# Performance work log

Measured on AMD Instinct MI355X. Metric: run time of the kernel, lower is better.

The kernel has to match this reference:

```python
import jax, jax.numpy as jnp
import numpy as np
import math

NUM_BUCKETS = 32
MAX_DISTANCE = 128

def _next_pow2(n):
    return 1 << (int(n) - 1).bit_length()

def _rel_pos_bucket(rel_pos):
    # causal T5 bucket: n = max(q - k, 0)
    n = jnp.maximum(-rel_pos, 0)
    max_exact = NUM_BUCKETS // 2
    is_small = n < max_exact
    n_safe = jnp.maximum(n, 1).astype(jnp.float32)
    val_if_large = max_exact + (
        jnp.log(n_safe / max_exact) / math.log(MAX_DISTANCE / max_exact) * (NUM_BUCKETS - max_exact)
    ).astype(jnp.int32)
    val_if_large = jnp.minimum(val_if_large, NUM_BUCKETS - 1)
    return jnp.where(is_small, n, val_if_large)

def setup_inputs() -> dict:
    key = jax.random.key(0)
    ks = jax.random.split(key, 20)
    B, L, D = 8, 2048, 128
    H, DQK, DV = 16, 64, 256
    s = 0.05
    return {
        'x': jax.random.normal(ks[0], (B, L, D), jnp.float32),
        'expansion': jax.random.normal(ks[1], (H, D), jnp.float32) * s,
        'reduction': jax.random.normal(ks[2], (H, D), jnp.float32) * s,
        'alphas': jax.random.normal(ks[3], (H,), jnp.float32),
        'dampen_factors': jax.random.normal(ks[4], (H,), jnp.float32),
        'rel_bias': jax.random.normal(ks[5], (NUM_BUCKETS, 1), jnp.float32) * s,
        'W_qk': jax.random.normal(ks[6], (D, DQK), jnp.float32) * s,
        'b_qk': jnp.zeros((DQK,), jnp.float32),
        'gamma': jax.random.normal(ks[7], (2, DQK), jnp.float32) * 0.02 + 1.0,
        'beta': jnp.zeros((2, DQK), jnp.float32),
        'W_v': jax.random.normal(ks[8], (D, DV), jnp.float32) * s,
        'b_v': jnp.zeros((DV,), jnp.float32),
        'W_reset': jax.random.normal(ks[9], (D, DV), jnp.float32) * s,
        'b_reset': jnp.zeros((DV,), jnp.float32),
        'W_update': jax.random.normal(ks[10], (D, D), jnp.float32) * s,
        'b_update': jnp.zeros((D,), jnp.float32),
        'Wh': jax.random.normal(ks[11], (D, D), jnp.float32) * s,
        'Uh': jax.random.normal(ks[12], (DV, D), jnp.float32) * s,
        'bh': jnp.zeros((D,), jnp.float32),
    }

def reference(x, expansion, reduction, alphas, dampen_factors, rel_bias,
              W_qk, b_qk, gamma, beta, W_v, b_v, W_reset, b_reset,
              W_update, b_update, Wh, Uh, bh):
    B, L, D = x.shape
    DQK = W_qk.shape[1]
    # ---- MultiHeadedEMA (causal, FFT conv) ----
    xe = jnp.einsum('bnd,hd->bnhd', x, expansion)  # [B,L,H,D]
    a = jax.nn.sigmoid(alphas)
    damp = jax.nn.sigmoid(dampen_factors)
    t = jnp.arange(L, dtype=x.dtype)
    kern = a[:, None] * ((1.0 - a) * damp)[:, None] ** t[None, :]  # [H,L]
    fft_len = _next_pow2(2 * L - 1)
    Xf = jnp.fft.rfft(xe, n=fft_len, axis=1)           # [B,F,H,D]
    Kf = jnp.fft.rfft(kern, n=fft_len, axis=-1)        # [H,F]
    y = jnp.fft.irfft(Xf * Kf.T[None, :, :, None], n=fft_len, axis=1)[:, :L]
    ema = jnp.einsum('bnhd,hd->bnd', y, reduction)     # [B,L,D]
    # ---- SingleHeadedAttention(ema, v_input=x) ----
    qk = jax.nn.silu(ema @ W_qk + b_qk)                # [B,L,DQK]
    q = qk * gamma[0] + beta[0]
    k = qk * gamma[1] + beta[1]
    v = jax.nn.silu(x @ W_v + b_v)                     # [B,L,DV]
    scale = D ** -0.5
    sim = jnp.einsum('bid,bjd->bij', q, k) * scale
    pos = jnp.arange(L)
    rel = pos[None, :] - pos[:, None]                  # [L,L] j - i
    bias = rel_bias[_rel_pos_bucket(rel), 0] * (DQK ** 0.5)
    sim = sim + bias
    sim = jnp.where(rel > 0, jnp.finfo(sim.dtype).min, sim)  # strict causal mask
    attn = jax.nn.softmax(sim, axis=-1)
    attn_out = jnp.einsum('bij,bjd->bid', attn, v)     # [B,L,DV]
    # ---- gating ----
    reset_gate = jax.nn.silu(ema @ W_reset + b_reset)
    update_gate = jax.nn.sigmoid(ema @ W_update + b_update)
    gated = attn_out * reset_gate
    Hh = jax.nn.silu(ema @ Wh + gated @ Uh + bh)
    return update_gate * Hh + (1.0 - update_gate) * x
```

## Files before the change

### kernel.cpp

```cpp
#include <hip/hip_runtime.h>
#include <hip/hip_bf16.h>
#include <math.h>

#define BB 8
#define LL 2048
#define DD 128
#define DQKN 64
#define DVN 256
#define MTOT (BB*LL)
#define SCALE 0.08838834764831845f
#define LOG2E 1.4426950408889634f
#define QSCALE (SCALE*LOG2E)

#define CHUNK 32
#define NCH (LL/CHUNK)
#define CT 4
#define NCHK 144

typedef __attribute__((ext_vector_type(4))) float f32x4;
typedef __attribute__((ext_vector_type(8))) short s16x8;

__device__ __forceinline__ float sigmoidf_(float x){ return 1.f/(1.f+__expf(-x)); }
__device__ __forceinline__ float siluf_(float x){ return x/(1.f+__expf(-x)); }
__device__ __forceinline__ __hip_bfloat16 f2bf(float f){ return __float2bfloat16(f); }
__device__ __forceinline__ ushort f2bfu(float f){ __hip_bfloat16 h = __float2bfloat16(f); return *(const ushort*)&h; }
__device__ __forceinline__ float bf2f(ushort u){ union{unsigned i; float f;} v; v.i = ((unsigned)u)<<16; return v.f; }

__device__ __forceinline__ void gl_lds16(const __hip_bfloat16* g, void* l) {
    __builtin_amdgcn_global_load_lds(
        (const __attribute__((address_space(1))) void*)g,
        (__attribute__((address_space(3))) void*)l, 16, 0, 0);
}

__global__ void pack_all(const float* __restrict__ Wqk, const float* __restrict__ Wv,
                         const float* __restrict__ Wrst, const float* __restrict__ Wu,
                         const float* __restrict__ Wh, const float* __restrict__ Uh,
                         const float* __restrict__ rel_bias,
                         __hip_bfloat16* __restrict__ WqkP, __hip_bfloat16* __restrict__ WvP,
                         __hip_bfloat16* __restrict__ WrstP, __hip_bfloat16* __restrict__ WuP,
                         __hip_bfloat16* __restrict__ WhP, __hip_bfloat16* __restrict__ UhP,
                         float* __restrict__ btab) {
    int blk = blockIdx.x;
    int l = threadIdx.x;
    if (blk == 272) {
        for (int n = l; n < LL; n += 64) {
            int bucket;
            if (n < 16) bucket = n;
            else {
                float v = logf((float)n * (1.0f/16.0f)) * (1.0f/logf(8.0f)) * 16.0f;
                bucket = 16 + (int)v;
                if (bucket > 31) bucket = 31;
            }
            btab[n] = rel_bias[bucket] * 8.0f * LOG2E;
        }
        return;
    }
    const float* W; __hip_bfloat16* Wp; int K, N;
    if (blk < 16)       { W=Wqk;  Wp=WqkP;  K=128; N=64; }
    else if (blk < 80)  { W=Wv;   Wp=WvP;   K=128; N=256; blk-=16; }
    else if (blk < 144) { W=Wrst; Wp=WrstP; K=128; N=256; blk-=80; }
    else if (blk < 176) { W=Wu;   Wp=WuP;   K=128; N=128; blk-=144; }
    else if (blk < 208) { W=Wh;   Wp=WhP;   K=128; N=128; blk-=176; }
    else                { W=Uh;   Wp=UhP;   K=256; N=128; blk-=208; }
    int k32 = blk % (K/32), n16 = blk / (K/32);
    int col = n16*16 + (l & 15);
    int krow = k32*32 + (l >> 4)*8;
    ushort tmp[8];
    #pragma unroll
    for (int j = 0; j < 8; ++j) tmp[j] = f2bfu(W[(size_t)(krow + j)*N + col]);
    *reinterpret_cast<uint4*>(Wp + ((size_t)blk*64 + l)*8) = *reinterpret_cast<uint4*>(tmp);
}

__global__ __launch_bounds__(256) void ema_scanA(const float* __restrict__ x,
                                                 const float* __restrict__ alphas,
                                                 const float* __restrict__ damps,
                                                 float* __restrict__ sl) {
    int tid = blockIdx.x * 256 + threadIdx.x;
    int d = tid & 127;
    int c = (tid >> 7) & (NCH - 1);
    int b = tid >> 13;
    float u[16], r[16];
    #pragma unroll
    for (int h = 0; h < 16; ++h) {
        float a = sigmoidf_(alphas[h]);
        r[h] = (1.f - a) * sigmoidf_(damps[h]);
        u[h] = 0.f;
    }
    const float* xp = x + ((size_t)b * LL + c * CHUNK) * DD + d;
    #pragma unroll 4
    for (int i = 0; i < CHUNK; ++i) {
        float xv = xp[(size_t)i * DD];
        #pragma unroll
        for (int h = 0; h < 16; ++h) u[h] = fmaf(r[h], u[h], xv);
    }
    float* slp = sl + ((size_t)b * NCH + c) * 16 * DD + d;
    #pragma unroll
    for (int h = 0; h < 16; ++h) slp[(size_t)h * DD] = u[h];
}

__global__ __launch_bounds__(256) void ema_scanB(const float* __restrict__ alphas,
                                                 const float* __restrict__ damps,
                                                 const float* __restrict__ sl,
                                                 float* __restrict__ carry) {
    int tid = blockIdx.x * 256 + threadIdx.x;
    int d = tid & 127;
    int h = (tid >> 7) & 15;
    int b = tid >> 11;
    float a = sigmoidf_(alphas[h]);
    float r = (1.f - a) * sigmoidf_(damps[h]);
    float rC = r;
    #pragma unroll
    for (int q = 0; q < 5; ++q) rC *= rC;
    const float* slp = sl + ((size_t)b * NCH * 16 + h) * DD + d;
    float* cp = carry + ((size_t)b * NCH * 16 + h) * DD + d;
    float u = 0.f;
    for (int c = 0; c < NCH; ++c) {
        cp[(size_t)c * 16 * DD] = u;
        u = slp[(size_t)c * 16 * DD] + rC * u;
    }
}

__global__ __launch_bounds__(256) void ema_scanC(const float* __restrict__ x,
                                                 const float* __restrict__ expansion,
                                                 const float* __restrict__ reduction,
                                                 const float* __restrict__ alphas,
                                                 const float* __restrict__ damps,
                                                 const float* __restrict__ carry,
                                                 __hip_bfloat16* __restrict__ emab,
                                                 __hip_bfloat16* __restrict__ xb) {
    int tid = blockIdx.x * 256 + threadIdx.x;
    int d = tid & 127;
    int c = (tid >> 7) & (NCH - 1);
    int b = tid >> 13;
    float u[16], r[16], we[16];
    #pragma unroll
    for (int h = 0; h < 16; ++h) {
        float a = sigmoidf_(alphas[h]);
        r[h] = (1.f - a) * sigmoidf_(damps[h]);
        we[h] = reduction[h * DD + d] * a * expansion[h * DD + d];
        u[h] = carry[((size_t)b * NCH + c) * 16 * DD + (size_t)h * DD + d];
    }
    const float* xp = x + ((size_t)b * LL + c * CHUNK) * DD + d;
    __hip_bfloat16* ep = emab + ((size_t)b * LL + c * CHUNK) * DD + d;
    __hip_bfloat16* xbp = xb + ((size_t)b * LL + c * CHUNK) * DD + d;
    #pragma unroll 4
    for (int i = 0; i < CHUNK; ++i) {
        float xv = xp[(size_t)i * DD];
        float acc = 0.f;
        #pragma unroll
        for (int h = 0; h < 16; ++h) {
            u[h] = fmaf(r[h], u[h], xv);
            acc = fmaf(we[h], u[h], acc);
        }
        ep[(size_t)i * DD] = f2bf(acc);
        xbp[(size_t)i * DD] = f2bf(xv);
    }
}

__global__ __launch_bounds__(256) void gemm_qk(const __hip_bfloat16* __restrict__ A,
        const __hip_bfloat16* __restrict__ Wp, const float* __restrict__ bias,
        const float* __restrict__ gamma, const float* __restrict__ beta,
        __hip_bfloat16* __restrict__ qb, __hip_bfloat16* __restrict__ kb) {
    __shared__ char AsB[64*256];
    const int row0 = blockIdx.x * 64;
    const int t = threadIdx.x, w = t>>6, lane = t&63, l16 = lane&15, l4 = lane>>4;
    #pragma unroll
    for (int p = 0; p < 4; ++p) {
        int idx = p*256 + t;
        int row = idx / 16, u = idx % 16;
        uint4 d = *reinterpret_cast<const uint4*>(A + (size_t)(row0+row)*DD + u*8);
        *reinterpret_cast<uint4*>(AsB + row*256 + ((u*16) ^ ((row&7)<<4))) = d;
    }
    __syncthreads();
    f32x4 acc[4];
    #pragma unroll
    for (int n = 0; n < 4; ++n) acc[n] = (f32x4){0.f,0.f,0.f,0.f};
    const int arow = w*16 + l16;
    #pragma unroll
    for (int k32 = 0; k32 < 4; ++k32) {
        s16x8 af = *reinterpret_cast<const s16x8*>(AsB + arow*256 + ((k32*64 + l4*16) ^ ((arow&7)<<4)));
        #pragma unroll
        for (int n = 0; n < 4; ++n) {
            s16x8 bfr = *reinterpret_cast<const s16x8*>(Wp + ((size_t)(n*4 + k32)*64 + lane)*8);
            acc[n] = __builtin_amdgcn_mfma_f32_16x16x32_bf16(af, bfr, acc[n], 0, 0, 0);
        }
    }
    #pragma unroll
    for (int n = 0; n < 4; ++n) {
        int col = n*16 + l16;
        float bb = bias[col];
        float g0 = gamma[col], g1 = gamma[DQKN + col];
        float be0 = beta[col], be1 = beta[DQKN + col];
        #pragma unroll
        for (int r = 0; r < 4; ++r) {
            int row = w*16 + l4*4 + r;
            float s = siluf_(acc[n][r] + bb);
            qb[(size_t)(row0+row)*DQKN + col] = f2bf((s*g0 + be0) * QSCALE);
            kb[(size_t)(row0+row)*DQKN + col] = f2bf(s*g1 + be1);
        }
    }
}

__global__ __launch_bounds__(256) void gemm_vrst(const __hip_bfloat16* __restrict__ xb,
        const __hip_bfloat16* __restrict__ emab,
        const __hip_bfloat16* __restrict__ WvP, const __hip_bfloat16* __restrict__ WrstP,
        const float* __restrict__ b_v, const float* __restrict__ b_rst,
        __hip_bfloat16* __restrict__ vT, __hip_bfloat16* __restrict__ rstb) {
    __shared__ char AsB[64*256];
    const int mode = blockIdx.y;
    const __hip_bfloat16* A = mode ? emab : xb;
    const __hip_bfloat16* Wp = mode ? WrstP : WvP;
    const float* bias = mode ? b_rst : b_v;
    const int row0 = blockIdx.x * 64;
    const int t = threadIdx.x, w = t>>6, lane = t&63, l16 = lane&15, l4 = lane>>4;
    #pragma unroll
    for (int p = 0; p < 4; ++p) {
        int idx = p*256 + t;
        int row = idx / 16, u = idx % 16;
        uint4 d = *reinterpret_cast<const uint4*>(A + (size_t)(row0+row)*DD + u*8);
        *reinterpret_cast<uint4*>(AsB + row*256 + ((u*16) ^ ((row&7)<<4))) = d;
    }
    __syncthreads();
    f32x4 acc[16];
    #pragma unroll
    for (int n = 0; n < 16; ++n) acc[n] = (f32x4){0.f,0.f,0.f,0.f};
    const int arow = w*16 + l16;
    #pragma unroll
    for (int k32 = 0; k32 < 4; ++k32) {
        s16x8 af = *reinterpret_cast<const s16x8*>(AsB + arow*256 + ((k32*64 + l4*16) ^ ((arow&7)<<4)));
        #pragma unroll
        for (int n = 0; n < 16; ++n) {
            s16x8 bfr = *reinterpret_cast<const s16x8*>(Wp + ((size_t)(n*4 + k32)*64 + lane)*8);
            acc[n] = __builtin_amdgcn_mfma_f32_16x16x32_bf16(af, bfr, acc[n], 0, 0, 0);
        }
    }
    if (mode == 0) {
        int bb_i = row0 >> 11;
        int lpos0 = (row0 & 2047) + w*16 + l4*4;
        #pragma unroll
        for (int n = 0; n < 16; ++n) {
            int col = n*16 + l16;
            float bb = bias[col];
            ushort pk[4];
            #pragma unroll
            for (int r = 0; r < 4; ++r) pk[r] = f2bfu(siluf_(acc[n][r] + bb));
            *reinterpret_cast<ushort4*>(vT + ((size_t)bb_i*DVN + col)*LL + lpos0) = *reinterpret_cast<ushort4*>(pk);
        }
    } else {
        #pragma unroll
        for (int n = 0; n < 16; ++n) {
            int col = n*16 + l16;
            float bb = bias[col];
            #pragma unroll
            for (int r = 0; r < 4; ++r) {
                int row = w*16 + l4*4 + r;
                rstb[(size_t)(row0+row)*DVN + col] = f2bf(siluf_(acc[n][r] + bb));
            }
        }
    }
}

__global__ __launch_bounds__(256) void attn_kernel(
    const __hip_bfloat16* __restrict__ qg, const __hip_bfloat16* __restrict__ kg,
    const __hip_bfloat16* __restrict__ vTg, const float* __restrict__ btab,
    __hip_bfloat16* __restrict__ aob, __hip_bfloat16* __restrict__ part_o,
    float* __restrict__ part_ml) {
    __shared__ __hip_bfloat16 Ks[2][64 * 64];
    __shared__ __hip_bfloat16 Vs[2][256 * 64];
    __shared__ __hip_bfloat16 Ps[4][16][72];
    __shared__ float btl[320];
    const int cid = NCHK - 1 - (int)blockIdx.x;
    const int b = blockIdx.y;
    int g = 0;
    while (cid >= 2*(g+1)*(g+2)) ++g;
    const int rel = cid - 2*g*(g+1);
    const int ti = 4*g + rel/(g+1);
    const int cch = rel % (g+1);
    const int i0 = ti * 64;
    const int jlo = cch * (CT*64);
    int jhi = jlo + CT*64; { int je = (ti+1)*64; if (jhi > je) jhi = je; }
    const int nt = (jhi - jlo) >> 6;
    const int t = threadIdx.x;
    const int w = t >> 6, lane = t & 63;
    const int l16 = lane & 15, l4 = lane >> 4;
    char* KsB = (char*)Ks;
    char* VsB = (char*)Vs;

    const int dminE = i0 - jhi + 1;
    const int cnt = (i0 + 63 - jlo) - dminE + 1;
    for (int idx = t; idx < cnt; idx += 256) {
        int dlt = dminE + idx;
        btl[idx] = (dlt >= 0) ? btab[dlt] : -1e30f;
    }

    const int irow = i0 + w * 16 + l16;
    s16x8 qf[2];
    qf[0] = *reinterpret_cast<const s16x8*>(qg + ((size_t)b * LL + irow) * DQKN + l4 * 8);
    qf[1] = *reinterpret_cast<const s16x8*>(qg + ((size_t)b * LL + irow) * DQKN + 32 + l4 * 8);

    f32x4 o[16];
    #pragma unroll
    for (int n16 = 0; n16 < 16; ++n16) o[n16] = (f32x4){0.f, 0.f, 0.f, 0.f};
    float m[4] = {-1e30f, -1e30f, -1e30f, -1e30f};
    float l[4] = {0.f, 0.f, 0.f, 0.f};

    #define STAGE(BUF, J0) { \
        _Pragma("unroll") for (int i = 0; i < 2; ++i) { \
            int base = w * 128 + i * 64; \
            int idx = base + lane; \
            int row = idx >> 3; \
            int c16 = (idx & 7) ^ (row & 7); \
            gl_lds16(kg + ((size_t)b * LL + (J0) + row) * DQKN + c16 * 8, KsB + (BUF)*8192 + base * 16); } \
        _Pragma("unroll") for (int i = 0; i < 8; ++i) { \
            int base = w * 512 + i * 64; \
            int idx = base + lane; \
            int n = idx >> 3; \
            int c16 = (idx & 7) ^ (n & 7); \
            gl_lds16(vTg + ((size_t)b * DVN + n) * LL + (J0) + c16 * 8, VsB + (BUF)*32768 + base * 16); } }

    STAGE(0, jlo);
    __syncthreads();

    for (int tt = 0; tt < nt; ++tt) {
        const int j0 = jlo + tt * 64;
        const int cur = tt & 1;
        if (tt + 1 < nt) STAGE(cur ^ 1, j0 + 64);
        f32x4 s[4];
        #pragma unroll
        for (int t16 = 0; t16 < 4; ++t16) s[t16] = (f32x4){0.f, 0.f, 0.f, 0.f};
        #pragma unroll
        for (int c = 0; c < 2; ++c) {
            #pragma unroll
            for (int t16 = 0; t16 < 4; ++t16) {
                int j = t16 * 16 + l16;
                s16x8 kf = *reinterpret_cast<const s16x8*>(KsB + cur*8192 + j * 128 + ((c * 64 + l4 * 16) ^ ((j & 7) << 4)));
                s[t16] = __builtin_amdgcn_mfma_f32_16x16x32_bf16(qf[c], kf, s[t16], 0, 0, 0);
            }
        }
        const int Cb = (i0 + w * 16 + l4 * 4) - (j0 + l16) - dminE;
        float sv[4][4];
        float rmax[4] = {-1e30f, -1e30f, -1e30f, -1e30f};
        #pragma unroll
        for (int t16 = 0; t16 < 4; ++t16) {
            #pragma unroll
            for (int r = 0; r < 4; ++r) {
                float val = s[t16][r] + btl[Cb + r - t16 * 16];
                sv[t16][r] = val;
                rmax[r] = fmaxf(rmax[r], val);
            }
        }
        #pragma unroll
        for (int off = 1; off < 16; off <<= 1) {
            #pragma unroll
            for (int r = 0; r < 4; ++r) rmax[r] = fmaxf(rmax[r], __shfl_xor(rmax[r], off));
        }
        bool need = (rmax[0] > m[0]) || (rmax[1] > m[1]) || (rmax[2] > m[2]) || (rmax[3] > m[3]);
        if (__any(need)) {
            float alpha[4];
            #pragma unroll
            for (int r = 0; r < 4; ++r) {
                float mn = fmaxf(m[r], rmax[r]);
                alpha[r] = exp2f(m[r] - mn);
                m[r] = mn;
                l[r] *= alpha[r];
            }
            #pragma unroll
            for (int n16 = 0; n16 < 16; ++n16) {
                #pragma unroll
                for (int r = 0; r < 4; ++r) o[n16][r] *= alpha[r];
            }
        }
        float psum[4] = {0.f, 0.f, 0.f, 0.f};
        #pragma unroll
        for (int t16 = 0; t16 < 4; ++t16) {
            #pragma unroll
            for (int r = 0; r < 4; ++r) {
                float p = exp2f(sv[t16][r] - m[r]);
                psum[r] += p;
                Ps[w][l4 * 4 + r][t16 * 16 + l16] = f2bf(p);
            }
        }
        #pragma unroll
        for (int off = 1; off < 16; off <<= 1) {
            #pragma unroll
            for (int r = 0; r < 4; ++r) psum[r] += __shfl_xor(psum[r], off);
        }
        #pragma unroll
        for (int r = 0; r < 4; ++r) l[r] += psum[r];
        #pragma unroll
        for (int c = 0; c < 2; ++c) {
            s16x8 pf = *reinterpret_cast<const s16x8*>(&Ps[w][l16][c * 32 + l4 * 8]);
            #pragma unroll
            for (int n16 = 0; n16 < 16; ++n16) {
                int n = n16 * 16 + l16;
                s16x8 vf = *reinterpret_cast<const s16x8*>(VsB + cur*32768 + n * 128 + ((c * 64 + l4 * 16) ^ ((n & 7) << 4)));
                o[n16] = __builtin_amdgcn_mfma_f32_16x16x32_bf16(pf, vf, o[n16], 0, 0, 0);
            }
        }
        __syncthreads();
    }
    #undef STAGE
    if (ti < 4) {
        float invl[4];
        #pragma unroll
        for (int r = 0; r < 4; ++r) invl[r] = 1.f / l[r];
        #pragma unroll
        for (int n16 = 0; n16 < 16; ++n16) {
            #pragma unroll
            for (int r = 0; r < 4; ++r) {
                aob[((size_t)b * LL + i0 + w * 16 + l4 * 4 + r) * DVN + n16 * 16 + l16] = f2bf(o[n16][r] * invl[r]);
            }
        }
    } else {
        const size_t slot = (size_t)b * NCHK + cid;
        __hip_bfloat16* po = part_o + slot * (64 * 256);
        #pragma unroll
        for (int n16 = 0; n16 < 16; ++n16) {
            #pragma unroll
            for (int r = 0; r < 4; ++r)
                po[(size_t)(w * 16 + l4 * 4 + r) * 256 + n16 * 16 + l16] = f2bf(o[n16][r]);
        }
        if (l16 == 0) {
            #pragma unroll
            for (int r = 0; r < 4; ++r) {
                int row = w * 16 + l4 * 4 + r;
                part_ml[slot * 128 + row * 2]     = m[r];
                part_ml[slot * 128 + row * 2 + 1] = l[r];
            }
        }
    }
}

__global__ __launch_bounds__(256) void attn_combine(const __hip_bfloat16* __restrict__ part_o,
                                                    const float* __restrict__ part_ml,
                                                    __hip_bfloat16* __restrict__ aob) {
    const int ti = 4 + (int)blockIdx.x;
    const int ch = blockIdx.y;
    const int b = blockIdx.z;
    const int g = ti >> 2;
    const int nc = g + 1;
    const int cid0 = 2*g*(g+1) + (ti - 4*g)*(g+1);
    const size_t slot0 = (size_t)b * NCHK + cid0;
    __shared__ float sW[8][64];
    __shared__ float sinvL[64];
    const int t = threadIdx.x;
    if (t < 64) {
        float M = -1e30f;
        for (int c = 0; c < nc; ++c)
            M = fmaxf(M, part_ml[(slot0 + c) * 128 + t * 2]);
        float L = 0.f;
        for (int c = 0; c < nc; ++c) {
            float wv = exp2f(part_ml[(slot0 + c) * 128 + t * 2] - M);
            sW[c][t] = wv;
            L += wv * part_ml[(slot0 + c) * 128 + t * 2 + 1];
        }
        sinvL[t] = 1.f / L;
    }
    __syncthreads();
    const int i0 = ti * 64;
    #pragma unroll
    for (int it = 0; it < 4; ++it) {
        int idx = it * 256 + t;
        int row = idx >> 4, c8 = idx & 15;
        int colu = ch * 16 + c8;
        float acc[8] = {0.f,0.f,0.f,0.f,0.f,0.f,0.f,0.f};
        for (int c = 0; c < nc; ++c) {
            float wv = sW[c][row];
            uint4 d = *reinterpret_cast<const uint4*>(part_o + (slot0 + c) * (size_t)(64*256) + row * 256 + colu * 8);
            const ushort* pp = (const ushort*)&d;
            #pragma unroll
            for (int j = 0; j < 8; ++j) acc[j] = fmaf(wv, bf2f(pp[j]), acc[j]);
        }
        float il = sinvL[row];
        ushort pk[8];
        #pragma unroll
        for (int j = 0; j < 8; ++j) pk[j] = f2bfu(acc[j] * il);
        *reinterpret_cast<uint4*>(aob + ((size_t)b * LL + i0 + row) * DVN + colu * 8) = *reinterpret_cast<uint4*>(pk);
    }
}

__global__ __launch_bounds__(256) void final_mfma(
        const __hip_bfloat16* __restrict__ emab, const __hip_bfloat16* __restrict__ aob,
        const __hip_bfloat16* __restrict__ rstb, const float* __restrict__ x,
        const __hip_bfloat16* __restrict__ WhP, const __hip_bfloat16* __restrict__ UhP,
        const __hip_bfloat16* __restrict__ WuP, const float* __restrict__ bh,
        const float* __restrict__ bu, float* __restrict__ out) {
    __shared__ char As1[64*256];
    __shared__ char As2[64*512];
    const int row0 = blockIdx.x * 64;
    const int ch = blockIdx.y;
    const int t = threadIdx.x, w = t>>6, lane = t&63, l16 = lane&15, l4 = lane>>4;
    #pragma unroll
    for (int p = 0; p < 4; ++p) {
        int idx = p*256 + t;
        int row = idx / 16, u = idx % 16;
        uint4 d = *reinterpret_cast<const uint4*>(emab + (size_t)(row0+row)*DD + u*8);
        *reinterpret_cast<uint4*>(As1 + row*256 + ((u*16) ^ ((row&7)<<4))) = d;
    }
    #pragma unroll
    for (int p = 0; p < 8; ++p) {
        int idx = p*256 + t;
        int row = idx / 32, u = idx % 32;
        uint4 da = *reinterpret_cast<const uint4*>(aob + (size_t)(row0+row)*DVN + u*8);
        uint4 dr = *reinterpret_cast<const uint4*>(rstb + (size_t)(row0+row)*DVN + u*8);
        const ushort* pa = (const ushort*)&da;
        const ushort* pr = (const ushort*)&dr;
        ushort gg[8];
        #pragma unroll
        for (int j = 0; j < 8; ++j) gg[j] = f2bfu(bf2f(pa[j]) * bf2f(pr[j]));
        *reinterpret_cast<uint4*>(As2 + row*512 + ((u*16) ^ ((row&7)<<4))) = *reinterpret_cast<uint4*>(gg);
    }
    __syncthreads();
    f32x4 acc1[4], acc2[4];
    #pragma unroll
    for (int n = 0; n < 4; ++n) { acc1[n] = (f32x4){0.f,0.f,0.f,0.f}; acc2[n] = (f32x4){0.f,0.f,0.f,0.f}; }
    const int arow = w*16 + l16;
    #pragma unroll
    for (int k32 = 0; k32 < 4; ++k32) {
        s16x8 af = *reinterpret_cast<const s16x8*>(As1 + arow*256 + ((k32*64 + l4*16) ^ ((arow&7)<<4)));
        #pragma unroll
        for (int n = 0; n < 4; ++n) {
            s16x8 bw = *reinterpret_cast<const s16x8*>(WhP + ((size_t)((ch*4+n)*4 + k32)*64 + lane)*8);
            acc1[n] = __builtin_amdgcn_mfma_f32_16x16x32_bf16(af, bw, acc1[n], 0, 0, 0);
            s16x8 bu2 = *reinterpret_cast<const s16x8*>(WuP + ((size_t)((ch*4+n)*4 + k32)*64 + lane)*8);
            acc2[n] = __builtin_amdgcn_mfma_f32_16x16x32_bf16(af, bu2, acc2[n], 0, 0, 0);
        }
    }
    #pragma unroll
    for (int k32 = 0; k32 < 8; ++k32) {
        s16x8 gf = *reinterpret_cast<const s16x8*>(As2 + arow*512 + ((k32*64 + l4*16) ^ ((arow&7)<<4)));
        #pragma unroll
        for (int n = 0; n < 4; ++n) {
            s16x8 bw = *reinterpret_cast<const s16x8*>(UhP + ((size_t)((ch*4+n)*8 + k32)*64 + lane)*8);
            acc1[n] = __builtin_amdgcn_mfma_f32_16x16x32_bf16(gf, bw, acc1[n], 0, 0, 0);
        }
    }
    #pragma unroll
    for (int n = 0; n < 4; ++n) {
        int col = ch*64 + n*16 + l16;
        float bbh = bh[col], bbu = bu[col];
        #pragma unroll
        for (int r = 0; r < 4; ++r) {
            int row = w*16 + l4*4 + r;
            size_t gidx = (size_t)(row0+row)*DD + col;
            float hh = siluf_(acc1[n][r] + bbh);
            float u = sigmoidf_(acc2[n][r] + bbu);
            float xv = x[gidx];
            out[gidx] = u*hh + (1.f-u)*xv;
        }
    }
}

extern "C" void kernel_launch(void* const* d_in, const int* in_sizes, int n_in,
                              void* d_out, int out_size, void* d_ws, size_t ws_size,
                              hipStream_t stream) {
    const float* x        = (const float*)d_in[0];
    const float* expansion= (const float*)d_in[1];
    const float* reduction= (const float*)d_in[2];
    const float* alphas   = (const float*)d_in[3];
    const float* damps    = (const float*)d_in[4];
    const float* rel_bias = (const float*)d_in[5];
    const float* W_qk     = (const float*)d_in[6];
    const float* b_qk     = (const float*)d_in[7];
    const float* gamma    = (const float*)d_in[8];
    const float* beta     = (const float*)d_in[9];
    const float* W_v      = (const float*)d_in[10];
    const float* b_v      = (const float*)d_in[11];
    const float* W_reset  = (const float*)d_in[12];
    const float* b_reset  = (const float*)d_in[13];
    const float* W_update = (const float*)d_in[14];
    const float* b_update = (const float*)d_in[15];
    const float* Wh       = (const float*)d_in[16];
    const float* Uh       = (const float*)d_in[17];
    const float* bh       = (const float*)d_in[18];
    float* out = (float*)d_out;

    char* base = (char*)d_ws;
    __hip_bfloat16* emab = (__hip_bfloat16*)base;  base += (size_t)MTOT * DD * 2;
    __hip_bfloat16* xb   = (__hip_bfloat16*)base;  base += (size_t)MTOT * DD * 2;
    __hip_bfloat16* qb   = (__hip_bfloat16*)base;  base += (size_t)MTOT * DQKN * 2;
    __hip_bfloat16* kb   = (__hip_bfloat16*)base;  base += (size_t)MTOT * DQKN * 2;
    __hip_bfloat16* vT   = (__hip_bfloat16*)base;  base += (size_t)MTOT * DVN * 2;
    __hip_bfloat16* rstb = (__hip_bfloat16*)base;  base += (size_t)MTOT * DVN * 2;
    __hip_bfloat16* aob  = (__hip_bfloat16*)base;  base += (size_t)MTOT * DVN * 2;
    float* btab  = (float*)base;                   base += (size_t)LL * 4;
    float* sl    = (float*)base;                   base += (size_t)BB * NCH * 16 * DD * 4;
    float* carry = (float*)base;                   base += (size_t)BB * NCH * 16 * DD * 4;
    __hip_bfloat16* WqkP = (__hip_bfloat16*)base;  base += (size_t)DD * DQKN * 2;
    __hip_bfloat16* WvP  = (__hip_bfloat16*)base;  base += (size_t)DD * DVN * 2;
    __hip_bfloat16* WrstP= (__hip_bfloat16*)base;  base += (size_t)DD * DVN * 2;
    __hip_bfloat16* WuP  = (__hip_bfloat16*)base;  base += (size_t)DD * DD * 2;
    __hip_bfloat16* WhP  = (__hip_bfloat16*)base;  base += (size_t)DD * DD * 2;
    __hip_bfloat16* UhP  = (__hip_bfloat16*)base;  base += (size_t)DVN * DD * 2;
    __hip_bfloat16* part_o = (__hip_bfloat16*)base; base += (size_t)BB * NCHK * 64 * 256 * 2;
    float* part_ml = (float*)base;                 base += (size_t)BB * NCHK * 128 * 4;

    pack_all<<<273, 64, 0, stream>>>(W_qk, W_v, W_reset, W_update, Wh, Uh, rel_bias,
                                     WqkP, WvP, WrstP, WuP, WhP, UhP, btab);

    ema_scanA<<<BB * NCH * DD / 256, 256, 0, stream>>>(x, alphas, damps, sl);
    ema_scanB<<<BB * 16 * DD / 256, 256, 0, stream>>>(alphas, damps, sl, carry);
    ema_scanC<<<BB * NCH * DD / 256, 256, 0, stream>>>(x, expansion, reduction, alphas, damps, carry, emab, xb);

    gemm_qk<<<MTOT/64, 256, 0, stream>>>(emab, WqkP, b_qk, gamma, beta, qb, kb);
    gemm_vrst<<<dim3(MTOT/64, 2), 256, 0, stream>>>(xb, emab, WvP, WrstP, b_v, b_reset, vT, rstb);

    attn_kernel<<<dim3(NCHK, BB), 256, 0, stream>>>(qb, kb, vT, btab, aob, part_o, part_ml);
    attn_combine<<<dim3(28, 2, BB), 256, 0, stream>>>(part_o, part_ml, aob);

    final_mfma<<<dim3(MTOT/64, 2), 256, 0, stream>>>(emab, aob, rstb, x, WhP, UhP, WuP, bh, b_update, out);
}
```

Baseline: 136.9 us.

## Single-buffer attention K/V tiles, lazy softmax rescale, MFMA row-sum

The attention kernel drops the double-buffered K/V shared-memory staging in favour of a single buffer with two barriers per tile. This shrinks LDS use from about 80KB to about 40KB, which may let more blocks share a CU, but it exposes global-load latency because loads no longer overlap compute. The softmax running max is now updated only when a new row max exceeds the old one by more than 8 in log2 units, skipping most output rescales, and the softmax row sums are computed with an extra MFMA against a ones vector instead of shuffle reductions. The EMA carry scan loop also gets an unroll pragma.

```diff
diff --git a/kernel.cpp b/kernel.cpp
--- a/kernel.cpp
+++ b/kernel.cpp
@@ -114,6 +114,7 @@
     const float* slp = sl + ((size_t)b * NCH * 16 + h) * DD + d;
     float* cp = carry + ((size_t)b * NCH * 16 + h) * DD + d;
     float u = 0.f;
+    #pragma unroll 8
     for (int c = 0; c < NCH; ++c) {
         cp[(size_t)c * 16 * DD] = u;
         u = slp[(size_t)c * 16 * DD] + rC * u;
@@ -265,8 +266,8 @@
     const __hip_bfloat16* __restrict__ vTg, const float* __restrict__ btab,
     __hip_bfloat16* __restrict__ aob, __hip_bfloat16* __restrict__ part_o,
     float* __restrict__ part_ml) {
-    __shared__ __hip_bfloat16 Ks[2][64 * 64];
-    __shared__ __hip_bfloat16 Vs[2][256 * 64];
+    __shared__ __hip_bfloat16 Ks[64 * 64];
+    __shared__ __hip_bfloat16 Vs[256 * 64];
     __shared__ __hip_bfloat16 Ps[4][16][72];
     __shared__ float btl[320];
     const int cid = NCHK - 1 - (int)blockIdx.x;
@@ -298,33 +299,35 @@
     qf[0] = *reinterpret_cast<const s16x8*>(qg + ((size_t)b * LL + irow) * DQKN + l4 * 8);
     qf[1] = *reinterpret_cast<const s16x8*>(qg + ((size_t)b * LL + irow) * DQKN + 32 + l4 * 8);
 
+    s16x8 ones;
+    #pragma unroll
+    for (int j = 0; j < 8; ++j) ones[j] = (short)0x3F80;
+
     f32x4 o[16];
     #pragma unroll
     for (int n16 = 0; n16 < 16; ++n16) o[n16] = (f32x4){0.f, 0.f, 0.f, 0.f};
     float m[4] = {-1e30f, -1e30f, -1e30f, -1e30f};
     float l[4] = {0.f, 0.f, 0.f, 0.f};
 
-    #define STAGE(BUF, J0) { \
+    #define STAGE(J0) { \
         _Pragma("unroll") for (int i = 0; i < 2; ++i) { \
             int base = w * 128 + i * 64; \
             int idx = base + lane; \
             int row = idx >> 3; \
             int c16 = (idx & 7) ^ (row & 7); \
-            gl_lds16(kg + ((size_t)b * LL + (J0) + row) * DQKN + c16 * 8, KsB + (BUF)*8192 + base * 16); } \
+            gl_lds16(kg + ((size_t)b * LL + (J0) + row) * DQKN + c16 * 8, KsB + base * 16); } \
         _Pragma("unroll") for (int i = 0; i < 8; ++i) { \
             int base = w * 512 + i * 64; \
             int idx = base + lane; \
             int n = idx >> 3; \
             int c16 = (idx & 7) ^ (n & 7); \
-            gl_lds16(vTg + ((size_t)b * DVN + n) * LL + (J0) + c16 * 8, VsB + (BUF)*32768 + base * 16); } }
-
-    STAGE(0, jlo);
-    __syncthreads();
+            gl_lds16(vTg + ((size_t)b * DVN + n) * LL + (J0) + c16 * 8, VsB + base * 16); } }
 
     for (int tt = 0; tt < nt; ++tt) {
         const int j0 = jlo + tt * 64;
-        const int cur = tt & 1;
-        if (tt + 1 < nt) STAGE(cur ^ 1, j0 + 64);
+        __syncthreads();
+        STAGE(j0);
+        __syncthreads();
         f32x4 s[4];
         #pragma unroll
         for (int t16 = 0; t16 < 4; ++t16) s[t16] = (f32x4){0.f, 0.f, 0.f, 0.f};
@@ -333,7 +336,7 @@
             #pragma unroll
             for (int t16 = 0; t16 < 4; ++t16) {
                 int j = t16 * 16 + l16;
-                s16x8 kf = *reinterpret_cast<const s16x8*>(KsB + cur*8192 + j * 128 + ((c * 64 + l4 * 16) ^ ((j & 7) << 4)));
+                s16x8 kf = *reinterpret_cast<const s16x8*>(KsB + j * 128 + ((c * 64 + l4 * 16) ^ ((j & 7) << 4)));
                 s[t16] = __builtin_amdgcn_mfma_f32_16x16x32_bf16(qf[c], kf, s[t16], 0, 0, 0);
             }
         }
@@ -354,7 +357,8 @@
             #pragma unroll
             for (int r = 0; r < 4; ++r) rmax[r] = fmaxf(rmax[r], __shfl_xor(rmax[r], off));
         }
-        bool need = (rmax[0] > m[0]) || (rmax[1] > m[1]) || (rmax[2] > m[2]) || (rmax[3] > m[3]);
+        bool need = (rmax[0] > m[0] + 8.f) || (rmax[1] > m[1] + 8.f) ||
+                    (rmax[2] > m[2] + 8.f) || (rmax[3] > m[3] + 8.f);
         if (__any(need)) {
             float alpha[4];
             #pragma unroll
@@ -370,34 +374,28 @@
                 for (int r = 0; r < 4; ++r) o[n16][r] *= alpha[r];
             }
         }
-        float psum[4] = {0.f, 0.f, 0.f, 0.f};
         #pragma unroll
         for (int t16 = 0; t16 < 4; ++t16) {
             #pragma unroll
             for (int r = 0; r < 4; ++r) {
                 float p = exp2f(sv[t16][r] - m[r]);
-                psum[r] += p;
                 Ps[w][l4 * 4 + r][t16 * 16 + l16] = f2bf(p);
             }
         }
-        #pragma unroll
-        for (int off = 1; off < 16; off <<= 1) {
-            #pragma unroll
-            for (int r = 0; r < 4; ++r) psum[r] += __shfl_xor(psum[r], off);
-        }
-        #pragma unroll
-        for (int r = 0; r < 4; ++r) l[r] += psum[r];
+        f32x4 lacc = (f32x4){0.f, 0.f, 0.f, 0.f};
         #pragma unroll
         for (int c = 0; c < 2; ++c) {
             s16x8 pf = *reinterpret_cast<const s16x8*>(&Ps[w][l16][c * 32 + l4 * 8]);
+            lacc = __builtin_amdgcn_mfma_f32_16x16x32_bf16(pf, ones, lacc, 0, 0, 0);
             #pragma unroll
             for (int n16 = 0; n16 < 16; ++n16) {
                 int n = n16 * 16 + l16;
-                s16x8 vf = *reinterpret_cast<const s16x8*>(VsB + cur*32768 + n * 128 + ((c * 64 + l4 * 16) ^ ((n & 7) << 4)));
+                s16x8 vf = *reinterpret_cast<const s16x8*>(VsB + n * 128 + ((c * 64 + l4 * 16) ^ ((n & 7) << 4)));
                 o[n16] = __builtin_amdgcn_mfma_f32_16x16x32_bf16(pf, vf, o[n16], 0, 0, 0);
             }
         }
-        __syncthreads();
+        #pragma unroll
+        for (int r = 0; r < 4; ++r) l[r] += lacc[r];
     }
     #undef STAGE
     if (ti < 4) {
```

New measurement: 128.7 us. -6.0%, faster.
